# Kernel tuning notes

Hardware: AMD Instinct MI355X
Metric: run time of the kernel (lower is better)

The kernel has to match this reference:

```python
import jax, jax.numpy as jnp
import numpy as np

N_NODES = 100000
N_EDGES = 1600000
IN_DIM = 128
HID = 128
HEADS = 8
NEG_SLOPE = 0.2  # PyG GATConv default


def _gat_layer(x, src, dst, W, a_src, a_dst, bias, heads, n_nodes):
    """One PyG-style GATConv (concat=True). src/dst already include self-loops."""
    out_ch = W.shape[1] // heads
    h = (x @ W).reshape(n_nodes, heads, out_ch)          # [N, H, C]
    alpha_s = jnp.sum(h * a_src, axis=-1)                # [N, H]
    alpha_d = jnp.sum(h * a_dst, axis=-1)                # [N, H]
    e = jax.nn.leaky_relu(alpha_s[src] + alpha_d[dst], negative_slope=NEG_SLOPE)  # [E, H]
    # segment softmax over destination nodes (stable; self-loops guarantee nonempty segments)
    m = jax.lax.stop_gradient(jax.ops.segment_max(e, dst, num_segments=n_nodes))
    ex = jnp.exp(e - m[dst])
    s = jax.ops.segment_sum(ex, dst, num_segments=n_nodes)
    alpha = ex / s[dst]                                  # [E, H]
    msg = h[src] * alpha[:, :, None]                     # [E, H, C]
    out = jax.ops.segment_sum(msg, dst, num_segments=n_nodes)  # [N, H, C]
    return out.reshape(n_nodes, heads * out_ch) + bias


def setup_inputs() -> dict:
    key = jax.random.key(0)
    ks = jax.random.split(key, 12)
    c1 = HID // HEADS  # per-head channels of layer 1
    g = lambda k, shape, fan_in: jax.random.normal(k, shape, dtype=jnp.float32) * (1.0 / np.sqrt(fan_in))
    return {
        "x": jax.random.normal(ks[0], (N_NODES, IN_DIM), dtype=jnp.float32),
        "edge_index": jax.random.randint(ks[1], (2, N_EDGES), 0, N_NODES, dtype=jnp.int32),
        "W1": g(ks[2], (IN_DIM, HEADS * c1), IN_DIM),
        "a_src1": g(ks[3], (HEADS, c1), c1),
        "a_dst1": g(ks[4], (HEADS, c1), c1),
        "b1": jnp.zeros((HEADS * c1,), dtype=jnp.float32),
        "W2": g(ks[5], (HID, HID), HID),
        "a_src2": g(ks[6], (1, HID), HID),
        "a_dst2": g(ks[7], (1, HID), HID),
        "b2": jnp.zeros((HID,), dtype=jnp.float32),
    }


def reference(x, edge_index, W1, a_src1, a_dst1, b1, W2, a_src2, a_dst2, b2):
    n = x.shape[0]
    loops = jnp.arange(n, dtype=edge_index.dtype)  # add_self_loops=True (PyG default)
    src = jnp.concatenate([edge_index[0], loops])
    dst = jnp.concatenate([edge_index[1], loops])
    h = _gat_layer(x, src, dst, W1, a_src1, a_dst1, b1, HEADS, n)
    h = jax.nn.elu(h)  # inter-layer ELU; dropout p=0.0 is a no-op
    out = _gat_layer(h, src, dst, W2, a_src2, a_dst2, b2, 1, n)
    return out
```

## Files before the change

### kernel.cpp

```cpp
#include <hip/hip_runtime.h>
#include <hip/hip_bf16.h>
#include <math.h>

#define NEG_SLOPE 0.2f

typedef _Float16 half8 __attribute__((ext_vector_type(8)));
typedef _Float16 half4 __attribute__((ext_vector_type(4)));
typedef float f32x4 __attribute__((ext_vector_type(4)));

__device__ __forceinline__ float lrelu(float x){ return x > 0.0f ? x : NEG_SLOPE * x; }

__global__ void hist_kernel(const int* __restrict__ dst, int E,
                            int* __restrict__ deg, int rangeSize){
  const int x   = blockIdx.x & 7;
  const int gb  = blockIdx.x >> 3;
  const int nGB = gridDim.x >> 3;
  const int lo = x * rangeSize, hi = lo + rangeSize;
  const int stride = nGB * blockDim.x;
  for (int i = gb * blockDim.x + threadIdx.x; i < E; i += stride){
    int d = dst[i];
    if (d >= lo && d < hi) atomicAdd(&deg[d], 1);
  }
}

__global__ void scan1_kernel(const int* __restrict__ deg, int N,
                             int* __restrict__ rowptr, int* __restrict__ bsum){
  __shared__ int sdata[256];
  int t = threadIdx.x;
  int base = blockIdx.x * 1024;
  int v[4];
  int run = 0;
#pragma unroll
  for (int j = 0; j < 4; ++j){
    int idx = base + t*4 + j;
    int d = (idx < N) ? deg[idx] : 0;
    run += d;
    v[j] = run;
  }
  sdata[t] = run;
  __syncthreads();
  for (int off = 1; off < 256; off <<= 1){
    int x = (t >= off) ? sdata[t - off] : 0;
    __syncthreads();
    sdata[t] += x;
    __syncthreads();
  }
  int prev = (t > 0) ? sdata[t-1] : 0;
#pragma unroll
  for (int j = 0; j < 4; ++j){
    int idx = base + t*4 + j;
    if (idx < N) rowptr[idx + 1] = v[j] + prev;
  }
  if (t == 255) bsum[blockIdx.x] = sdata[255];
}

__global__ void scan2_kernel(int* __restrict__ bsum, int nb){
  if (threadIdx.x == 0 && blockIdx.x == 0){
    int run = 0;
    for (int i = 0; i < nb; ++i){ int x = bsum[i]; bsum[i] = run; run += x; }
  }
}

__global__ void scan3_kernel(int* __restrict__ rowptr, const int* __restrict__ bsum, int N){
  int i = blockIdx.x * blockDim.x + threadIdx.x;
  if (i == 0) rowptr[0] = 0;
  if (i < N) rowptr[i + 1] += bsum[i >> 10];
}

__global__ void scatter_kernel(const int* __restrict__ src, const int* __restrict__ dst, int E,
                               const int* __restrict__ rowptr, int* __restrict__ fill,
                               int* __restrict__ csr_src, int rangeSize){
  const int x   = blockIdx.x & 7;
  const int gb  = blockIdx.x >> 3;
  const int nGB = gridDim.x >> 3;
  const int lo = x * rangeSize, hi = lo + rangeSize;
  const int stride = nGB * blockDim.x;
  for (int i = gb * blockDim.x + threadIdx.x; i < E; i += stride){
    int d = dst[i];
    if (d >= lo && d < hi){
      int pos = rowptr[d] + atomicAdd(&fill[d], 1);
      csr_src[pos] = src[i];
    }
  }
}

__global__ void prep_kernel(const float* __restrict__ W1, const float* __restrict__ W2,
                            const float* __restrict__ as2, const float* __restrict__ ad2,
                            _Float16* __restrict__ Wt1, _Float16* __restrict__ Wt2,
                            float* __restrict__ w2s, float* __restrict__ w2d){
  int t = threadIdx.x;
  if (blockIdx.x < 2){
    const float* W = blockIdx.x ? W2 : W1;
    _Float16* Wt = blockIdx.x ? Wt2 : Wt1;
    for (int i = 0; i < 64; ++i){
      int e = i*256 + t;
      int k = e >> 7, c = e & 127;
      Wt[c*128 + k] = (_Float16)W[e];
    }
  } else {
    if (t < 128){
      float ps = 0.f, pd = 0.f;
      for (int c = 0; c < 128; ++c){
        float w = W2[t*128 + c];
        ps += w * as2[c];
        pd += w * ad2[c];
      }
      w2s[t] = ps;
      w2d[t] = pd;
    }
  }
}

template<int ALPHA_H, bool CASTF32, bool OUTF32>
__launch_bounds__(256, 2)
__global__ void gemm_mfma(const void* __restrict__ Aptr, const _Float16* __restrict__ Wt,
                          void* __restrict__ outp, const float* __restrict__ bias,
                          const float* __restrict__ a_src, const float* __restrict__ a_dst,
                          float* __restrict__ alpha_s, float* __restrict__ alpha_d, int N){
  __shared__ __align__(16) _Float16 Xs[128*128];
  __shared__ __align__(16) _Float16 Ws[128*128];
  __shared__ float apart[2][128][2];
  const int t = threadIdx.x;
  const int lane = t & 63;
  const int w = t >> 6;
  const int wr = w & 1, wc = w >> 1;
  const int rowBase = blockIdx.x * 128;
  const int lrow = lane & 15, lk = lane >> 4;

  if (CASTF32){
    const float* A = (const float*)Aptr;
#pragma unroll
    for (int p = 0; p < 16; ++p){
      int flat = p*256 + t;
      int row = flat >> 5, seg = flat & 31;
      int gr = rowBase + row;
      float4 v = (gr < N) ? *(const float4*)(A + (size_t)gr*128 + seg*4)
                          : make_float4(0.f,0.f,0.f,0.f);
      half4 hv = {(_Float16)v.x, (_Float16)v.y, (_Float16)v.z, (_Float16)v.w};
      int byt = (row*256 + seg*8) ^ ((row & 7) << 4);
      *(half4*)((char*)Xs + byt) = hv;
    }
  } else {
    const _Float16* A = (const _Float16*)Aptr;
#pragma unroll
    for (int p = 0; p < 8; ++p){
      int flat = p*256 + t;
      int row = flat >> 4, seg = flat & 15;
      int gr = rowBase + row;
      int4 v = (gr < N) ? *(const int4*)(A + (size_t)gr*128 + seg*8)
                        : make_int4(0,0,0,0);
      int byt = (row*256 + seg*16) ^ ((row & 7) << 4);
      *(int4*)((char*)Xs + byt) = v;
    }
  }
#pragma unroll
  for (int p = 0; p < 8; ++p){
    int flat = p*256 + t;
    int row = flat >> 4, seg = flat & 15;
    int4 v = *(const int4*)(Wt + row*128 + seg*8);
    int byt = (row*256 + seg*16) ^ ((row & 7) << 4);
    *(int4*)((char*)Ws + byt) = v;
  }
  __syncthreads();

  f32x4 acc[4][4];
#pragma unroll
  for (int mf = 0; mf < 4; ++mf)
#pragma unroll
    for (int nf = 0; nf < 4; ++nf) acc[mf][nf] = (f32x4){0.f,0.f,0.f,0.f};

#pragma unroll
  for (int ks = 0; ks < 4; ++ks){
    const int kbyte = ks*64 + lk*16;
    half8 b[4], a[4];
#pragma unroll
    for (int nf = 0; nf < 4; ++nf){
      int row = wr*64 + nf*16 + lrow;
      b[nf] = *(const half8*)((const char*)Xs + ((row*256 + kbyte) ^ ((row & 7) << 4)));
    }
#pragma unroll
    for (int mf = 0; mf < 4; ++mf){
      int col = wc*64 + mf*16 + lrow;
      a[mf] = *(const half8*)((const char*)Ws + ((col*256 + kbyte) ^ ((col & 7) << 4)));
    }
#pragma unroll
    for (int mf = 0; mf < 4; ++mf)
#pragma unroll
      for (int nf = 0; nf < 4; ++nf)
        acc[mf][nf] = __builtin_amdgcn_mfma_f32_16x16x32_f16(a[mf], b[nf], acc[mf][nf], 0, 0, 0);
  }

  if (OUTF32){
    float* outf = (float*)outp;
    float4 b4[4];
#pragma unroll
    for (int mf = 0; mf < 4; ++mf)
      b4[mf] = *(const float4*)(bias + wc*64 + mf*16 + lk*4);
#pragma unroll
    for (int nf = 0; nf < 4; ++nf){
      int row = rowBase + wr*64 + nf*16 + lrow;
      if (row < N){
#pragma unroll
        for (int mf = 0; mf < 4; ++mf){
          int col = wc*64 + mf*16 + lk*4;
          f32x4 v = acc[mf][nf];
          float4 st = make_float4(v.x + b4[mf].x, v.y + b4[mf].y, v.z + b4[mf].z, v.w + b4[mf].w);
          *(float4*)(outf + (size_t)row*128 + col) = st;
        }
      }
    }
  } else {
    _Float16* hout = (_Float16*)outp;
#pragma unroll
    for (int nf = 0; nf < 4; ++nf){
      int row = rowBase + wr*64 + nf*16 + lrow;
      if (row < N){
#pragma unroll
        for (int mf = 0; mf < 4; ++mf){
          int col = wc*64 + mf*16 + lk*4;
          f32x4 v = acc[mf][nf];
          half4 hv = {(_Float16)v.x, (_Float16)v.y, (_Float16)v.z, (_Float16)v.w};
          *(half4*)(hout + (size_t)row*128 + col) = hv;
        }
      }
    }
  }

  if (ALPHA_H > 0){
    float4 as4[4], ad4[4];
#pragma unroll
    for (int mf = 0; mf < 4; ++mf){
      int cb = wc*64 + mf*16 + lk*4;
      as4[mf] = *(const float4*)(a_src + cb);
      ad4[mf] = *(const float4*)(a_dst + cb);
    }
    if (ALPHA_H == 8){
#pragma unroll
      for (int nf = 0; nf < 4; ++nf){
        int row = rowBase + wr*64 + nf*16 + lrow;
#pragma unroll
        for (int mf = 0; mf < 4; ++mf){
          f32x4 v = acc[mf][nf];
          float ps = v.x*as4[mf].x + v.y*as4[mf].y + v.z*as4[mf].z + v.w*as4[mf].w;
          float pd = v.x*ad4[mf].x + v.y*ad4[mf].y + v.z*ad4[mf].z + v.w*ad4[mf].w;
          ps += __shfl_xor(ps, 16); ps += __shfl_xor(ps, 32);
          pd += __shfl_xor(pd, 16); pd += __shfl_xor(pd, 32);
          if (lane < 16 && row < N){
            int head = wc*4 + mf;
            alpha_s[(size_t)row*8 + head] = ps;
            alpha_d[(size_t)row*8 + head] = pd;
          }
        }
      }
    } else {
#pragma unroll
      for (int nf = 0; nf < 4; ++nf){
        float ps = 0.f, pd = 0.f;
#pragma unroll
        for (int mf = 0; mf < 4; ++mf){
          f32x4 v = acc[mf][nf];
          ps += v.x*as4[mf].x + v.y*as4[mf].y + v.z*as4[mf].z + v.w*as4[mf].w;
          pd += v.x*ad4[mf].x + v.y*ad4[mf].y + v.z*ad4[mf].z + v.w*ad4[mf].w;
        }
        ps += __shfl_xor(ps, 16); ps += __shfl_xor(ps, 32);
        pd += __shfl_xor(pd, 16); pd += __shfl_xor(pd, 32);
        if (lane < 16){
          int rl = wr*64 + nf*16 + lane;
          apart[0][rl][wc] = ps;
          apart[1][rl][wc] = pd;
        }
      }
      __syncthreads();
      if (wc == 0){
        int rl = wr*64 + lane;
        int row = rowBase + rl;
        if (row < N){
          alpha_s[row] = apart[0][rl][0] + apart[0][rl][1];
          alpha_d[row] = apart[1][rl][0] + apart[1][rl][1];
        }
      }
    }
  }
}

template<int H, bool LAYER1>
__launch_bounds__(256)
__global__ void agg_kernel(const _Float16* __restrict__ hb, const float* __restrict__ alpha_s,
                           const float* __restrict__ alpha_d,
                           const int* __restrict__ rowptr, const int* __restrict__ csr_src,
                           const float* __restrict__ bias,
                           const float* __restrict__ w2s, const float* __restrict__ w2d,
                           _Float16* __restrict__ outh,
                           float* __restrict__ as2, float* __restrict__ ad2, int N){
  int wid = threadIdx.x >> 6, lane = threadIdx.x & 63;
  int n = blockIdx.x * 4 + wid;
  if (n >= N) return;
  int start = rowptr[n];
  int deg = rowptr[n + 1] - start;

  const int g  = lane >> 4;
  const int l  = lane & 15;
  const int ch = l * 8;
  const int hm = (H == 8) ? (l >> 1) : 0;
  const float ad_m = alpha_d[(size_t)n*H + hm];

  float acc[8];
#pragma unroll
  for (int i = 0; i < 8; ++i) acc[i] = 0.f;
  float ssum = 0.f;

  if (g == 3){
    float ex = __expf(lrelu(alpha_s[(size_t)n*H + hm] + ad_m));
    half8 hv = *(const half8*)(hb + (size_t)n*128 + ch);
#pragma unroll
    for (int i = 0; i < 8; ++i) acc[i] += (float)hv[i] * ex;
    ssum += ex;
  }

  int i = g;
  for (; i + 4 < deg; i += 8){
    int s0 = csr_src[start + i];
    int s1 = csr_src[start + i + 4];
    float a0 = alpha_s[(size_t)s0*H + hm];
    float a1 = alpha_s[(size_t)s1*H + hm];
    half8 h0 = *(const half8*)(hb + (size_t)s0*128 + ch);
    half8 h1 = *(const half8*)(hb + (size_t)s1*128 + ch);
    float e0 = __expf(lrelu(a0 + ad_m));
    float e1 = __expf(lrelu(a1 + ad_m));
#pragma unroll
    for (int k = 0; k < 8; ++k) acc[k] += (float)h0[k] * e0;
#pragma unroll
    for (int k = 0; k < 8; ++k) acc[k] += (float)h1[k] * e1;
    ssum += e0 + e1;
  }
  if (i < deg){
    int s0 = csr_src[start + i];
    float a0 = alpha_s[(size_t)s0*H + hm];
    half8 h0 = *(const half8*)(hb + (size_t)s0*128 + ch);
    float e0 = __expf(lrelu(a0 + ad_m));
#pragma unroll
    for (int k = 0; k < 8; ++k) acc[k] += (float)h0[k] * e0;
    ssum += e0;
  }

#pragma unroll
  for (int off = 16; off < 64; off <<= 1){
    ssum += __shfl_xor(ssum, off);
#pragma unroll
    for (int k = 0; k < 8; ++k) acc[k] += __shfl_xor(acc[k], off);
  }

  if (lane < 16){
    float inv = 1.0f / ssum;
    float o[8];
    if (LAYER1){
      float4 b0 = *(const float4*)(bias + ch);
      float4 b1 = *(const float4*)(bias + ch + 4);
      float bb[8] = {b0.x,b0.y,b0.z,b0.w,b1.x,b1.y,b1.z,b1.w};
#pragma unroll
      for (int k = 0; k < 8; ++k){
        float v = acc[k]*inv + bb[k];
        o[k] = (v > 0.f) ? v : expm1f(v);
      }
    } else {
#pragma unroll
      for (int k = 0; k < 8; ++k) o[k] = acc[k]*inv;
    }
    half8 ho;
#pragma unroll
    for (int k = 0; k < 8; ++k) ho[k] = (_Float16)o[k];
    *(half8*)(outh + (size_t)n*128 + ch) = ho;

    if (LAYER1){
      float4 s0 = *(const float4*)(w2s + ch);
      float4 s1 = *(const float4*)(w2s + ch + 4);
      float4 d0 = *(const float4*)(w2d + ch);
      float4 d1 = *(const float4*)(w2d + ch + 4);
      float ps = o[0]*s0.x + o[1]*s0.y + o[2]*s0.z + o[3]*s0.w
               + o[4]*s1.x + o[5]*s1.y + o[6]*s1.z + o[7]*s1.w;
      float pd = o[0]*d0.x + o[1]*d0.y + o[2]*d0.z + o[3]*d0.w
               + o[4]*d1.x + o[5]*d1.y + o[6]*d1.z + o[7]*d1.w;
#pragma unroll
      for (int off = 1; off < 16; off <<= 1){
        ps += __shfl_xor(ps, off);
        pd += __shfl_xor(pd, off);
      }
      if (l == 0){
        as2[n] = ps;
        ad2[n] = pd;
      }
    }
  }
}

extern "C" void kernel_launch(void* const* d_in, const int* in_sizes, int n_in,
                              void* d_out, int out_size, void* d_ws, size_t ws_size,
                              hipStream_t stream){
  const float* x      = (const float*)d_in[0];
  const int*   ei     = (const int*)  d_in[1];
  const float* W1     = (const float*)d_in[2];
  const float* a_src1 = (const float*)d_in[3];
  const float* a_dst1 = (const float*)d_in[4];
  const float* b1     = (const float*)d_in[5];
  const float* W2     = (const float*)d_in[6];
  const float* a_src2 = (const float*)d_in[7];
  const float* a_dst2 = (const float*)d_in[8];
  const float* b2     = (const float*)d_in[9];
  float* out = (float*)d_out;

  const int N = in_sizes[0] / 128;
  const int E = in_sizes[1] / 2;
  const int* src = ei;
  const int* dst = ei + E;

  char* ws = (char*)d_ws;
  size_t off = 0;
  auto alloc = [&](size_t bytes) -> void* {
    void* p = ws + off;
    off += (bytes + 255) & ~(size_t)255;
    return p;
  };
  _Float16* hb   = (_Float16*)alloc((size_t)N * 128 * 2);
  _Float16* act  = (_Float16*)alloc((size_t)N * 128 * 2);
  float* asb     = (float*)alloc((size_t)N * 8 * 4);
  float* adb     = (float*)alloc((size_t)N * 8 * 4);
  float* as2     = (float*)alloc((size_t)N * 4);
  float* ad2     = (float*)alloc((size_t)N * 4);
  _Float16* Wt1  = (_Float16*)alloc(16384 * 2);
  _Float16* Wt2  = (_Float16*)alloc(16384 * 2);
  float* w2s     = (float*)alloc(128 * 4);
  float* w2d     = (float*)alloc(128 * 4);
  int*   csr     = (int*)  alloc((size_t)E * 4);
  int*   rowptr  = (int*)  alloc((size_t)(N + 1) * 4);
  int*   deg     = (int*)  alloc((size_t)N * 4);
  int*   fill    = (int*)  alloc((size_t)N * 4);
  int*   bsum    = (int*)  alloc(4096);

  hipMemsetAsync(deg, 0, (size_t)((char*)bsum - (char*)deg), stream);

  const int nb = (N + 1023) / 1024;
  const int rangeSize = (N + 7) / 8;
  prep_kernel   <<<3, 256, 0, stream>>>(W1, W2, a_src2, a_dst2, Wt1, Wt2, w2s, w2d);
  hist_kernel   <<<2048, 256, 0, stream>>>(dst, E, deg, rangeSize);
  scan1_kernel  <<<nb, 256, 0, stream>>>(deg, N, rowptr, bsum);
  scan2_kernel  <<<1, 64, 0, stream>>>(bsum, nb);
  scan3_kernel  <<<(N + 255)/256, 256, 0, stream>>>(rowptr, bsum, N);
  scatter_kernel<<<2048, 256, 0, stream>>>(src, dst, E, rowptr, fill, csr, rangeSize);

  const int gBlocks  = (N + 127) / 128;
  const int nBlocks4 = (N + 3) / 4;

  gemm_mfma<8, true, false><<<gBlocks, 256, 0, stream>>>(
      x, Wt1, hb, nullptr, a_src1, a_dst1, asb, adb, N);
  agg_kernel<8, true><<<nBlocks4, 256, 0, stream>>>(
      hb, asb, adb, rowptr, csr, b1, w2s, w2d, act, as2, ad2, N);
  agg_kernel<1, false><<<nBlocks4, 256, 0, stream>>>(
      act, as2, ad2, rowptr, csr, nullptr, nullptr, nullptr, hb, nullptr, nullptr, N);
  gemm_mfma<0, false, true><<<gBlocks, 256, 0, stream>>>(
      hb, Wt2, out, b2, nullptr, nullptr, nullptr, nullptr, N);
}
```

Before: 371.4 us.

## Cooperatively compute edge weights then shuffle-broadcast in aggregation; use cursor-based CSR scatter

The aggregation kernel now splits each chunk into two phases. First, lanes cooperatively load source indices and compute exp(leaky_relu) attention weights once per (edge, head), including the self-loop as an extra edge. Then each lane-group broadcasts those values with shuffles while it gathers the feature rows, so the same edge's alpha_s and exponential are no longer recomputed redundantly across lanes. The CSR build replaces rowptr-plus-fill atomics with a single cursor array initialised from the scan, which drops one load per edge and shrinks the memset. The cost is extra shuffles, and the unrolled two-edge loop is gone, which reduces memory-level parallelism in the gather.

```diff
diff --git a/kernel.cpp b/kernel.cpp
--- a/kernel.cpp
+++ b/kernel.cpp
@@ -6,9 +6,10 @@
 
 typedef _Float16 half8 __attribute__((ext_vector_type(8)));
 typedef _Float16 half4 __attribute__((ext_vector_type(4)));
+typedef _Float16 half2v __attribute__((ext_vector_type(2)));
 typedef float f32x4 __attribute__((ext_vector_type(4)));
 
-__device__ __forceinline__ float lrelu(float x){ return x > 0.0f ? x : NEG_SLOPE * x; }
+__device__ __forceinline__ float lrelu(float x){ return fmaxf(x, NEG_SLOPE * x); }
 
 __global__ void hist_kernel(const int* __restrict__ dst, int E,
                             int* __restrict__ deg, int rangeSize){
@@ -61,15 +62,19 @@
   }
 }
 
-__global__ void scan3_kernel(int* __restrict__ rowptr, const int* __restrict__ bsum, int N){
+__global__ void scan3_kernel(int* __restrict__ rowptr, const int* __restrict__ bsum,
+                             int* __restrict__ cursor, int N){
   int i = blockIdx.x * blockDim.x + threadIdx.x;
-  if (i == 0) rowptr[0] = 0;
-  if (i < N) rowptr[i + 1] += bsum[i >> 10];
+  if (i == 0){ rowptr[0] = 0; cursor[0] = 0; }
+  if (i < N){
+    int v = rowptr[i + 1] + bsum[i >> 10];
+    rowptr[i + 1] = v;
+    cursor[i + 1] = v;
+  }
 }
 
 __global__ void scatter_kernel(const int* __restrict__ src, const int* __restrict__ dst, int E,
-                               const int* __restrict__ rowptr, int* __restrict__ fill,
-                               int* __restrict__ csr_src, int rangeSize){
+                               int* __restrict__ cursor, int* __restrict__ csr_src, int rangeSize){
   const int x   = blockIdx.x & 7;
   const int gb  = blockIdx.x >> 3;
   const int nGB = gridDim.x >> 3;
@@ -78,7 +83,7 @@
   for (int i = gb * blockDim.x + threadIdx.x; i < E; i += stride){
     int d = dst[i];
     if (d >= lo && d < hi){
-      int pos = rowptr[d] + atomicAdd(&fill[d], 1);
+      int pos = atomicAdd(&cursor[d], 1);
       csr_src[pos] = src[i];
     }
   }
@@ -292,79 +297,88 @@
                            const float* __restrict__ w2s, const float* __restrict__ w2d,
                            _Float16* __restrict__ outh,
                            float* __restrict__ as2, float* __restrict__ ad2, int N){
-  int wid = threadIdx.x >> 6, lane = threadIdx.x & 63;
-  int n = blockIdx.x * 4 + wid;
+  const int wid = threadIdx.x >> 6, lane = threadIdx.x & 63;
+  const int n = blockIdx.x * 4 + wid;
   if (n >= N) return;
-  int start = rowptr[n];
-  int deg = rowptr[n + 1] - start;
+  const int start = rowptr[n];
+  const int deg = rowptr[n + 1] - start;
+  const int T = deg + 1;
 
   const int g  = lane >> 4;
   const int l  = lane & 15;
   const int ch = l * 8;
   const int hm = (H == 8) ? (l >> 1) : 0;
-  const float ad_m = alpha_d[(size_t)n*H + hm];
+
+  const int p1e = (H == 8) ? (lane >> 3) : lane;
+  const int p1h = (H == 8) ? (lane & 7) : 0;
+  const int CH  = (H == 8) ? 8 : 64;
+
+  const float ad1 = alpha_d[(size_t)n*H + p1h];
 
   float acc[8];
 #pragma unroll
-  for (int i = 0; i < 8; ++i) acc[i] = 0.f;
-  float ssum = 0.f;
-
-  if (g == 3){
-    float ex = __expf(lrelu(alpha_s[(size_t)n*H + hm] + ad_m));
-    half8 hv = *(const half8*)(hb + (size_t)n*128 + ch);
-#pragma unroll
-    for (int i = 0; i < 8; ++i) acc[i] += (float)hv[i] * ex;
-    ssum += ex;
-  }
-
-  int i = g;
-  for (; i + 4 < deg; i += 8){
-    int s0 = csr_src[start + i];
-    int s1 = csr_src[start + i + 4];
-    float a0 = alpha_s[(size_t)s0*H + hm];
-    float a1 = alpha_s[(size_t)s1*H + hm];
-    half8 h0 = *(const half8*)(hb + (size_t)s0*128 + ch);
-    half8 h1 = *(const half8*)(hb + (size_t)s1*128 + ch);
-    float e0 = __expf(lrelu(a0 + ad_m));
-    float e1 = __expf(lrelu(a1 + ad_m));
-#pragma unroll
-    for (int k = 0; k < 8; ++k) acc[k] += (float)h0[k] * e0;
-#pragma unroll
-    for (int k = 0; k < 8; ++k) acc[k] += (float)h1[k] * e1;
-    ssum += e0 + e1;
-  }
-  if (i < deg){
-    int s0 = csr_src[start + i];
-    float a0 = alpha_s[(size_t)s0*H + hm];
-    half8 h0 = *(const half8*)(hb + (size_t)s0*128 + ch);
-    float e0 = __expf(lrelu(a0 + ad_m));
-#pragma unroll
-    for (int k = 0; k < 8; ++k) acc[k] += (float)h0[k] * e0;
-    ssum += e0;
-  }
-
-#pragma unroll
-  for (int off = 16; off < 64; off <<= 1){
-    ssum += __shfl_xor(ssum, off);
-#pragma unroll
-    for (int k = 0; k < 8; ++k) acc[k] += __shfl_xor(acc[k], off);
+  for (int k = 0; k < 8; ++k) acc[k] = 0.f;
+  float ssum_l = 0.f;
+
+  for (int base = 0; base < T; base += CH){
+    int j = base + p1e;
+    float exf = 0.f;
+    int sv = n;
+    if (j < T){
+      if (j < deg) sv = csr_src[start + j];
+      float e = alpha_s[(size_t)sv*H + p1h] + ad1;
+      e = fmaxf(e, NEG_SLOPE * e);
+      exf = __expf(e);
+      ssum_l += exf;
+    }
+    int lim  = min(CH, T - base);
+    int limr = (lim + 3) & ~3;
+    for (int jj = g; jj < limr; jj += 4){
+      int srcl = (H == 8) ? (jj*8 + hm) : jj;
+      int s = __shfl(sv, srcl);
+      float ex = __shfl(exf, srcl);
+      int4 hv = *(const int4*)(hb + (s << 7) + ch);
+      half2v h0 = __builtin_bit_cast(half2v, hv.x);
+      half2v h1 = __builtin_bit_cast(half2v, hv.y);
+      half2v h2 = __builtin_bit_cast(half2v, hv.z);
+      half2v h3 = __builtin_bit_cast(half2v, hv.w);
+      acc[0] += (float)h0.x * ex; acc[1] += (float)h0.y * ex;
+      acc[2] += (float)h1.x * ex; acc[3] += (float)h1.y * ex;
+      acc[4] += (float)h2.x * ex; acc[5] += (float)h2.y * ex;
+      acc[6] += (float)h3.x * ex; acc[7] += (float)h3.y * ex;
+    }
+  }
+
+  if (H == 8){
+    ssum_l += __shfl_xor(ssum_l, 8);
+    ssum_l += __shfl_xor(ssum_l, 16);
+    ssum_l += __shfl_xor(ssum_l, 32);
+  } else {
+#pragma unroll
+    for (int off = 1; off < 64; off <<= 1) ssum_l += __shfl_xor(ssum_l, off);
+  }
+  float ssum = __shfl(ssum_l, hm);
+
+#pragma unroll
+  for (int k = 0; k < 8; ++k){
+    acc[k] += __shfl_xor(acc[k], 16);
+    acc[k] += __shfl_xor(acc[k], 32);
   }
 
   if (lane < 16){
     float inv = 1.0f / ssum;
     float o[8];
+#pragma unroll
+    for (int k = 0; k < 8; ++k) o[k] = acc[k] * inv;
     if (LAYER1){
       float4 b0 = *(const float4*)(bias + ch);
       float4 b1 = *(const float4*)(bias + ch + 4);
       float bb[8] = {b0.x,b0.y,b0.z,b0.w,b1.x,b1.y,b1.z,b1.w};
 #pragma unroll
       for (int k = 0; k < 8; ++k){
-        float v = acc[k]*inv + bb[k];
+        float v = o[k] + bb[k];
         o[k] = (v > 0.f) ? v : expm1f(v);
       }
-    } else {
-#pragma unroll
-      for (int k = 0; k < 8; ++k) o[k] = acc[k]*inv;
     }
     half8 ho;
 #pragma unroll
@@ -432,11 +446,11 @@
   float* w2d     = (float*)alloc(128 * 4);
   int*   csr     = (int*)  alloc((size_t)E * 4);
   int*   rowptr  = (int*)  alloc((size_t)(N + 1) * 4);
+  int*   cursor  = (int*)  alloc((size_t)(N + 1) * 4);
   int*   deg     = (int*)  alloc((size_t)N * 4);
-  int*   fill    = (int*)  alloc((size_t)N * 4);
   int*   bsum    = (int*)  alloc(4096);
 
-  hipMemsetAsync(deg, 0, (size_t)((char*)bsum - (char*)deg), stream);
+  hipMemsetAsync(deg, 0, (size_t)N * 4, stream);
 
   const int nb = (N + 1023) / 1024;
   const int rangeSize = (N + 7) / 8;
@@ -444,8 +458,8 @@
   hist_kernel   <<<2048, 256, 0, stream>>>(dst, E, deg, rangeSize);
   scan1_kernel  <<<nb, 256, 0, stream>>>(deg, N, rowptr, bsum);
   scan2_kernel  <<<1, 64, 0, stream>>>(bsum, nb);
-  scan3_kernel  <<<(N + 255)/256, 256, 0, stream>>>(rowptr, bsum, N);
-  scatter_kernel<<<2048, 256, 0, stream>>>(src, dst, E, rowptr, fill, csr, rangeSize);
+  scan3_kernel  <<<(N + 255)/256, 256, 0, stream>>>(rowptr, bsum, cursor, N);
+  scatter_kernel<<<2048, 256, 0, stream>>>(src, dst, E, cursor, csr, rangeSize);
 
   const int gBlocks  = (N + 127) / 128;
   const int nBlocks4 = (N + 3) / 4;
```

Result: slower. 390.5 us (+5.1%).
